# Optimization experiments

Measured on AMD Instinct MI355X. Metric: run time of the kernel, lower is better.

Reference implementation:

```python
import jax, jax.numpy as jnp
import numpy as np

# H36M parent-child joint pairs (the second assignment in the source overrides the first)
PARENT = np.array([[0,1],[1,2],[2,3],[0,4],[4,5],[5,6],[0,8],[8,14],[14,15],[15,16],[8,11],[11,12],[12,13],[8,10]])
NUM_JOINTS = 17
NUM_PAIRS = 14
GRID = 64


def create_heatmap(joint2d, size):
    # Gaussian with cov = 2*I evaluated on integer grid, normalized by its max.
    # Original: grid[i, j] = N([i, j]; mean=[x, y], 2I) / max -> pdf constant cancels.
    xy = joint2d * 64.0  # (B, J, 2)
    ii = jnp.arange(size, dtype=joint2d.dtype)
    dx = ii[None, None, :, None] - xy[..., 0][..., None, None]  # (B, J, size, 1)
    dy = ii[None, None, None, :] - xy[..., 1][..., None, None]  # (B, J, 1, size)
    d2 = dx * dx + dy * dy  # (B, J, size, size)
    g = jnp.exp(-d2 / 4.0)  # exp(-d2 / (2*var)), var = 2
    return g / jnp.max(g, axis=(2, 3), keepdims=True)


def setup_inputs() -> dict:
    key = jax.random.key(0)
    k1, k2, k3, k4 = jax.random.split(key, 4)
    B = 256
    return {
        "pred": jax.random.normal(k1, (B, NUM_JOINTS, 3), dtype=jnp.float32),
        "joints": jax.random.normal(k2, (B, NUM_JOINTS, 3), dtype=jnp.float32),
        "middle_out": jax.random.normal(k3, (B, NUM_JOINTS + 3 * NUM_PAIRS, GRID, GRID), dtype=jnp.float32),
        "joint2d": jax.random.uniform(k4, (B, NUM_JOINTS, 2), dtype=jnp.float32),
    }


def reference(pred, joints, middle_out, joint2d):
    eps = 0.1
    B, _, H, W = middle_out.shape
    # l3D: joints last dim == 3 branch
    l3d = jnp.mean(jnp.sum(jnp.abs(joints - pred[:, :NUM_JOINTS, :]), axis=(1, 2)))

    heatmap = create_heatmap(joint2d, H)  # (B, 17, 64, 64)

    # L2D: mean over batch of sum over joints of squared Frobenius norm (detached in original)
    diff = middle_out[:, :NUM_JOINTS] - heatmap
    L2D = jnp.mean(jnp.sum(jnp.sum(diff * diff, axis=(2, 3)), axis=1))

    # LHEM: vectorized heatmap triplets over batch and all 14 parent/child pairs
    p_idx = PARENT[:, 0]
    c_idx = PARENT[:, 1]
    hp = heatmap[:, p_idx]  # (B, 14, 64, 64)
    hc = heatmap[:, c_idx]  # (B, 14, 64, 64)
    d = joints[:, p_idx, 2] - joints[:, c_idx, 2]  # (B, 14)
    r = jnp.where(d > eps, 1, jnp.where(jnp.abs(d) < eps, 0, -1))[..., None, None]
    ch0 = jnp.where(r == -1, hc, 0.0)
    ch1 = jnp.where(r == 0, hp + hc, hp)
    ch2 = jnp.where(r == 1, hc, 0.0)
    T_GT = jnp.stack((ch0, ch1, ch2), axis=2)  # (B, 14, 3, 64, 64)
    T_pred = middle_out[:, NUM_JOINTS:NUM_JOINTS + 3 * NUM_PAIRS].reshape(B, NUM_PAIRS, 3, H, W)
    norms = jnp.sqrt(jnp.sum((T_GT - T_pred) ** 2, axis=(3, 4)))  # (B, 14, 3)
    LHEM = jnp.mean(jnp.sum(jnp.sum(norms, axis=2) ** 2, axis=1))

    Lint = 0.005 * (LHEM + L2D)
    # Original computes L2D / LHEM in detached numpy -> no gradient through Lint
    return l3d + jax.lax.stop_gradient(Lint)
```

## Files before the change

### kernel.cpp

```cpp
#include <hip/hip_runtime.h>
#include <math.h>

#define NJ 17
#define NP 14
#define NCH 59
#define BATCH 256

__constant__ int c_par0[NP] = {0, 1, 2, 0, 4, 5, 0, 8, 14, 15, 8, 11, 12, 8};
__constant__ int c_par1[NP] = {1, 2, 3, 4, 5, 6, 8, 14, 15, 16, 11, 12, 13, 10};

__global__ __launch_bounds__(256) void slice_sum_kernel(
    const float* __restrict__ joints,
    const float* __restrict__ middle,
    const float* __restrict__ joint2d,
    float* __restrict__ partial)
{
    const int c   = blockIdx.x;
    const int b   = blockIdx.y;
    const int tid = threadIdx.x;

    float wp = 0.f, wc = 0.f;
    int jp = 0, jc = 0;
    if (c < NJ) {
        jp = c; wp = 1.f;
    } else {
        const int pi = c - NJ;
        const int p  = pi / 3;
        const int ch = pi - p * 3;
        jp = c_par0[p];
        jc = c_par1[p];
        const float dz = joints[(b * NJ + jp) * 3 + 2] - joints[(b * NJ + jc) * 3 + 2];
        const int r = (dz > 0.1f) ? 1 : ((fabsf(dz) < 0.1f) ? 0 : -1);
        if (ch == 0)      { wp = 0.f; wc = (r == -1) ? 1.f : 0.f; }
        else if (ch == 1) { wp = 1.f; wc = (r ==  0) ? 1.f : 0.f; }
        else              { wp = 0.f; wc = (r ==  1) ? 1.f : 0.f; }
    }

    float xp = 0.f, yp = 0.f, mp = 0.f;
    float xq = 0.f, yq = 0.f, mq = 0.f;
    if (wp != 0.f) {
        xp = joint2d[(b * NJ + jp) * 2 + 0] * 64.f;
        yp = joint2d[(b * NJ + jp) * 2 + 1] * 64.f;
        const float rx = fminf(fmaxf(floorf(xp + 0.5f), 0.f), 63.f);
        const float ry = fminf(fmaxf(floorf(yp + 0.5f), 0.f), 63.f);
        mp = (rx - xp) * (rx - xp) + (ry - yp) * (ry - yp);
    }
    if (wc != 0.f) {
        xq = joint2d[(b * NJ + jc) * 2 + 0] * 64.f;
        yq = joint2d[(b * NJ + jc) * 2 + 1] * 64.f;
        const float rx = fminf(fmaxf(floorf(xq + 0.5f), 0.f), 63.f);
        const float ry = fminf(fmaxf(floorf(yq + 0.5f), 0.f), 63.f);
        mq = (rx - xq) * (rx - xq) + (ry - yq) * (ry - yq);
    }

    const float4* __restrict__ src =
        (const float4*)(middle + ((size_t)b * NCH + c) * 4096);

    float acc = 0.f;
    #pragma unroll
    for (int v = 0; v < 4; ++v) {
        const int idx  = tid + v * 256;
        const float4 m4 = src[idx];
        const int cell = idx * 4;
        const float fi = (float)(cell >> 6);
        const float k0 = (float)(cell & 63);
        const float mv[4] = {m4.x, m4.y, m4.z, m4.w};
        #pragma unroll
        for (int q = 0; q < 4; ++q) {
            const float fk = k0 + (float)q;
            float tgt = 0.f;
            if (wp != 0.f) {
                const float dx = fi - xp, dy = fk - yp;
                tgt += __expf(-0.25f * (dx * dx + dy * dy - mp));
            }
            if (wc != 0.f) {
                const float dx = fi - xq, dy = fk - yq;
                tgt += __expf(-0.25f * (dx * dx + dy * dy - mq));
            }
            const float d = tgt - mv[q];
            acc += d * d;
        }
    }

    #pragma unroll
    for (int off = 32; off > 0; off >>= 1)
        acc += __shfl_down(acc, off, 64);

    __shared__ float sred[4];
    if ((tid & 63) == 0) sred[tid >> 6] = acc;
    __syncthreads();
    if (tid == 0)
        partial[b * NCH + c] = sred[0] + sred[1] + sred[2] + sred[3];
}

__global__ __launch_bounds__(1024) void finalize_kernel(
    const float* __restrict__ pred,
    const float* __restrict__ joints,
    const float* __restrict__ partial,
    float* __restrict__ out)
{
    const int tid = threadIdx.x;
    double a = 0.0;

    for (int i = tid; i < BATCH * NJ * 3; i += 1024)
        a += (double)fabsf(joints[i] - pred[i]);

    double s2 = 0.0;

    for (int i = tid; i < BATCH * NJ; i += 1024) {
        const int b = i / NJ;
        const int c = i - b * NJ;
        s2 += (double)partial[b * NCH + c];
    }

    for (int i = tid; i < BATCH * NP; i += 1024) {
        const int b = i / NP;
        const int p = i - b * NP;
        const float* s = partial + b * NCH + NJ + p * 3;
        const float n = sqrtf(s[0]) + sqrtf(s[1]) + sqrtf(s[2]);
        s2 += (double)n * (double)n;
    }

    a += 0.005 * s2;

    __shared__ double sh[1024];
    sh[tid] = a;
    __syncthreads();
    #pragma unroll
    for (int off = 512; off > 0; off >>= 1) {
        if (tid < off) sh[tid] += sh[tid + off];
        __syncthreads();
    }
    if (tid == 0) out[0] = (float)(sh[0] * (1.0 / 256.0));
}

extern "C" void kernel_launch(void* const* d_in, const int* in_sizes, int n_in,
                              void* d_out, int out_size, void* d_ws, size_t ws_size,
                              hipStream_t stream) {
    const float* pred    = (const float*)d_in[0];
    const float* joints  = (const float*)d_in[1];
    const float* middle  = (const float*)d_in[2];
    const float* joint2d = (const float*)d_in[3];
    float* out     = (float*)d_out;
    float* partial = (float*)d_ws;

    dim3 grid(NCH, BATCH);
    slice_sum_kernel<<<grid, 256, 0, stream>>>(joints, middle, joint2d, partial);
    finalize_kernel<<<1, 1024, 0, stream>>>(pred, joints, partial, out);
}
```

Measured before the change: 340.9 us.

## Fuse finalize into main kernel with atomic accumulation and per-pair blocks

Merges the separate finalize kernel into the main kernel: each block adds its scaled contribution to a global double accumulator, and the last block (tracked with an atomic counter) writes the output. Triplet blocks now process all three channels of a pair together, so the two Gaussians are computed once per cell rather than once per channel, and the grid shrinks from 59 to 31 blocks per batch item. The l3D term is folded into the first block of each batch row. This adds a memset launch and about 8k atomics on one address, and the summation order now depends on block scheduling, so results are not bitwise deterministic.

```diff
diff --git a/kernel.cpp b/kernel.cpp
--- a/kernel.cpp
+++ b/kernel.cpp
@@ -5,133 +5,151 @@
 #define NP 14
 #define NCH 59
 #define BATCH 256
+#define GRIDX (NJ + NP)
+#define TOTAL_BLOCKS (GRIDX * BATCH)
 
 __constant__ int c_par0[NP] = {0, 1, 2, 0, 4, 5, 0, 8, 14, 15, 8, 11, 12, 8};
 __constant__ int c_par1[NP] = {1, 2, 3, 4, 5, 6, 8, 14, 15, 16, 11, 12, 13, 10};
 
-__global__ __launch_bounds__(256) void slice_sum_kernel(
+__device__ __forceinline__ void heat_params(const float* __restrict__ joint2d,
+                                            int b, int j,
+                                            float& x, float& y, float& m) {
+    x = joint2d[(b * NJ + j) * 2 + 0] * 64.f;
+    y = joint2d[(b * NJ + j) * 2 + 1] * 64.f;
+    const float rx = fminf(fmaxf(floorf(x + 0.5f), 0.f), 63.f);
+    const float ry = fminf(fmaxf(floorf(y + 0.5f), 0.f), 63.f);
+    m = (rx - x) * (rx - x) + (ry - y) * (ry - y);
+}
+
+__device__ __forceinline__ float wave_reduce(float v) {
+    #pragma unroll
+    for (int off = 32; off; off >>= 1) v += __shfl_down(v, off, 64);
+    return v;
+}
+
+__global__ __launch_bounds__(256) void fused_loss_kernel(
+    const float* __restrict__ pred,
     const float* __restrict__ joints,
     const float* __restrict__ middle,
     const float* __restrict__ joint2d,
-    float* __restrict__ partial)
+    float* __restrict__ out,
+    double* __restrict__ acc,
+    unsigned* __restrict__ counter)
 {
-    const int c   = blockIdx.x;
+    const int cb  = blockIdx.x;
     const int b   = blockIdx.y;
     const int tid = threadIdx.x;
 
-    float wp = 0.f, wc = 0.f;
-    int jp = 0, jc = 0;
-    if (c < NJ) {
-        jp = c; wp = 1.f;
+    __shared__ float sred[4][3];
+    float contrib = 0.f;
+
+    if (cb < NJ) {
+        float x, y, msh;
+        heat_params(joint2d, b, cb, x, y, msh);
+        const float4* __restrict__ src =
+            (const float4*)(middle + ((size_t)b * NCH + cb) * 4096);
+        float S = 0.f;
+        #pragma unroll
+        for (int v = 0; v < 4; ++v) {
+            const int idx  = tid + v * 256;
+            const float4 m4 = src[idx];
+            const int cell = idx * 4;
+            const float fi = (float)(cell >> 6);
+            const float k0 = (float)(cell & 63);
+            const float mv[4] = {m4.x, m4.y, m4.z, m4.w};
+            #pragma unroll
+            for (int q = 0; q < 4; ++q) {
+                const float dx = fi - x, dy = (k0 + (float)q) - y;
+                const float h = __expf(-0.25f * (dx * dx + dy * dy - msh));
+                const float d = h - mv[q];
+                S += d * d;
+            }
+        }
+        S = wave_reduce(S);
+        if ((tid & 63) == 0) sred[tid >> 6][0] = S;
+        __syncthreads();
+        if (tid == 0)
+            contrib = (0.005f / BATCH) *
+                      (sred[0][0] + sred[1][0] + sred[2][0] + sred[3][0]);
     } else {
-        const int pi = c - NJ;
-        const int p  = pi / 3;
-        const int ch = pi - p * 3;
-        jp = c_par0[p];
-        jc = c_par1[p];
-        const float dz = joints[(b * NJ + jp) * 3 + 2] - joints[(b * NJ + jc) * 3 + 2];
+        const int p  = cb - NJ;
+        const int jp = c_par0[p], jc = c_par1[p];
+        float xp, yp, mp, xc, yc, mc;
+        heat_params(joint2d, b, jp, xp, yp, mp);
+        heat_params(joint2d, b, jc, xc, yc, mc);
+        const float dz = joints[(b * NJ + jp) * 3 + 2] -
+                         (float)joints[(b * NJ + jc) * 3 + 2];
         const int r = (dz > 0.1f) ? 1 : ((fabsf(dz) < 0.1f) ? 0 : -1);
-        if (ch == 0)      { wp = 0.f; wc = (r == -1) ? 1.f : 0.f; }
-        else if (ch == 1) { wp = 1.f; wc = (r ==  0) ? 1.f : 0.f; }
-        else              { wp = 0.f; wc = (r ==  1) ? 1.f : 0.f; }
-    }
+        const float wc0 = (r == -1) ? 1.f : 0.f;
+        const float wc1 = (r ==  0) ? 1.f : 0.f;
+        const float wc2 = (r ==  1) ? 1.f : 0.f;
 
-    float xp = 0.f, yp = 0.f, mp = 0.f;
-    float xq = 0.f, yq = 0.f, mq = 0.f;
-    if (wp != 0.f) {
-        xp = joint2d[(b * NJ + jp) * 2 + 0] * 64.f;
-        yp = joint2d[(b * NJ + jp) * 2 + 1] * 64.f;
-        const float rx = fminf(fmaxf(floorf(xp + 0.5f), 0.f), 63.f);
-        const float ry = fminf(fmaxf(floorf(yp + 0.5f), 0.f), 63.f);
-        mp = (rx - xp) * (rx - xp) + (ry - yp) * (ry - yp);
-    }
-    if (wc != 0.f) {
-        xq = joint2d[(b * NJ + jc) * 2 + 0] * 64.f;
-        yq = joint2d[(b * NJ + jc) * 2 + 1] * 64.f;
-        const float rx = fminf(fmaxf(floorf(xq + 0.5f), 0.f), 63.f);
-        const float ry = fminf(fmaxf(floorf(yq + 0.5f), 0.f), 63.f);
-        mq = (rx - xq) * (rx - xq) + (ry - yq) * (ry - yq);
-    }
+        const float4* __restrict__ s0 =
+            (const float4*)(middle + ((size_t)b * NCH + NJ + p * 3) * 4096);
+        const float4* __restrict__ s1 = s0 + 1024;
+        const float4* __restrict__ s2 = s0 + 2048;
 
-    const float4* __restrict__ src =
-        (const float4*)(middle + ((size_t)b * NCH + c) * 4096);
-
-    float acc = 0.f;
-    #pragma unroll
-    for (int v = 0; v < 4; ++v) {
-        const int idx  = tid + v * 256;
-        const float4 m4 = src[idx];
-        const int cell = idx * 4;
-        const float fi = (float)(cell >> 6);
-        const float k0 = (float)(cell & 63);
-        const float mv[4] = {m4.x, m4.y, m4.z, m4.w};
+        float S0 = 0.f, S1 = 0.f, S2 = 0.f;
         #pragma unroll
-        for (int q = 0; q < 4; ++q) {
-            const float fk = k0 + (float)q;
-            float tgt = 0.f;
-            if (wp != 0.f) {
-                const float dx = fi - xp, dy = fk - yp;
-                tgt += __expf(-0.25f * (dx * dx + dy * dy - mp));
+        for (int v = 0; v < 4; ++v) {
+            const int idx = tid + v * 256;
+            const float4 m0 = s0[idx];
+            const float4 m1 = s1[idx];
+            const float4 m2 = s2[idx];
+            const int cell = idx * 4;
+            const float fi = (float)(cell >> 6);
+            const float k0 = (float)(cell & 63);
+            const float a0[4] = {m0.x, m0.y, m0.z, m0.w};
+            const float a1[4] = {m1.x, m1.y, m1.z, m1.w};
+            const float a2[4] = {m2.x, m2.y, m2.z, m2.w};
+            #pragma unroll
+            for (int q = 0; q < 4; ++q) {
+                const float fk = k0 + (float)q;
+                const float dxp = fi - xp, dyp = fk - yp;
+                const float hp = __expf(-0.25f * (dxp * dxp + dyp * dyp - mp));
+                const float dxc = fi - xc, dyc = fk - yc;
+                const float hc = __expf(-0.25f * (dxc * dxc + dyc * dyc - mc));
+                const float d0 = wc0 * hc - a0[q];
+                const float d1 = hp + wc1 * hc - a1[q];
+                const float d2 = wc2 * hc - a2[q];
+                S0 += d0 * d0; S1 += d1 * d1; S2 += d2 * d2;
             }
-            if (wc != 0.f) {
-                const float dx = fi - xq, dy = fk - yq;
-                tgt += __expf(-0.25f * (dx * dx + dy * dy - mq));
-            }
-            const float d = tgt - mv[q];
-            acc += d * d;
+        }
+        S0 = wave_reduce(S0); S1 = wave_reduce(S1); S2 = wave_reduce(S2);
+        if ((tid & 63) == 0) {
+            const int w = tid >> 6;
+            sred[w][0] = S0; sred[w][1] = S1; sred[w][2] = S2;
+        }
+        __syncthreads();
+        if (tid == 0) {
+            const float t0 = sred[0][0] + sred[1][0] + sred[2][0] + sred[3][0];
+            const float t1 = sred[0][1] + sred[1][1] + sred[2][1] + sred[3][1];
+            const float t2 = sred[0][2] + sred[1][2] + sred[2][2] + sred[3][2];
+            const float n = sqrtf(t0) + sqrtf(t1) + sqrtf(t2);
+            contrib = (0.005f / BATCH) * n * n;
         }
     }
 
-    #pragma unroll
-    for (int off = 32; off > 0; off >>= 1)
-        acc += __shfl_down(acc, off, 64);
-
-    __shared__ float sred[4];
-    if ((tid & 63) == 0) sred[tid >> 6] = acc;
-    __syncthreads();
-    if (tid == 0)
-        partial[b * NCH + c] = sred[0] + sred[1] + sred[2] + sred[3];
-}
-
-__global__ __launch_bounds__(1024) void finalize_kernel(
-    const float* __restrict__ pred,
-    const float* __restrict__ joints,
-    const float* __restrict__ partial,
-    float* __restrict__ out)
-{
-    const int tid = threadIdx.x;
-    double a = 0.0;
-
-    for (int i = tid; i < BATCH * NJ * 3; i += 1024)
-        a += (double)fabsf(joints[i] - pred[i]);
-
-    double s2 = 0.0;
-
-    for (int i = tid; i < BATCH * NJ; i += 1024) {
-        const int b = i / NJ;
-        const int c = i - b * NJ;
-        s2 += (double)partial[b * NCH + c];
+    if (cb == 0 && tid < 64) {
+        float v = 0.f;
+        if (tid < NJ * 3) {
+            const int i = b * NJ * 3 + tid;
+            v = fabsf(joints[i] - pred[i]);
+        }
+        v = wave_reduce(v);
+        if (tid == 0) contrib += v * (1.0f / BATCH);
     }
 
-    for (int i = tid; i < BATCH * NP; i += 1024) {
-        const int b = i / NP;
-        const int p = i - b * NP;
-        const float* s = partial + b * NCH + NJ + p * 3;
-        const float n = sqrtf(s[0]) + sqrtf(s[1]) + sqrtf(s[2]);
-        s2 += (double)n * (double)n;
+    if (tid == 0) {
+        atomicAdd(acc, (double)contrib);
+        __threadfence();
+        const unsigned old = atomicAdd(counter, 1u);
+        if (old == (unsigned)(TOTAL_BLOCKS - 1)) {
+            __threadfence();
+            const double v = atomicAdd(acc, 0.0);
+            out[0] = (float)v;
+        }
     }
-
-    a += 0.005 * s2;
-
-    __shared__ double sh[1024];
-    sh[tid] = a;
-    __syncthreads();
-    #pragma unroll
-    for (int off = 512; off > 0; off >>= 1) {
-        if (tid < off) sh[tid] += sh[tid + off];
-        __syncthreads();
-    }
-    if (tid == 0) out[0] = (float)(sh[0] * (1.0 / 256.0));
 }
 
 extern "C" void kernel_launch(void* const* d_in, const int* in_sizes, int n_in,
@@ -141,10 +159,14 @@
     const float* joints  = (const float*)d_in[1];
     const float* middle  = (const float*)d_in[2];
     const float* joint2d = (const float*)d_in[3];
-    float* out     = (float*)d_out;
-    float* partial = (float*)d_ws;
+    float* out = (float*)d_out;
 
-    dim3 grid(NCH, BATCH);
-    slice_sum_kernel<<<grid, 256, 0, stream>>>(joints, middle, joint2d, partial);
-    finalize_kernel<<<1, 1024, 0, stream>>>(pred, joints, partial, out);
+    double*   acc     = (double*)d_ws;
+    unsigned* counter = (unsigned*)((char*)d_ws + 8);
+
+    hipMemsetAsync(d_ws, 0, 16, stream);
+
+    dim3 grid(GRIDX, BATCH);
+    fused_loss_kernel<<<grid, 256, 0, stream>>>(pred, joints, middle, joint2d,
+                                                out, acc, counter);
 }
```

New measurement: 716.1 us. +110.0%, slower.
